# Kernel tuning notes

Hardware: AMD Instinct MI355X
Metric: run time of the kernel (lower is better)

## Reference

```python
import jax, jax.numpy as jnp
import numpy as np

T, HID = 2048, 4096
H = 32                 # num_heads
Q_LORA = 1536
KV_LORA = 512
D_NOPE = 128
D_ROPE = 64
D_QK = D_NOPE + D_ROPE  # 192
D_V = 128
EPS = 1e-6
THETA = 10000.0


def rmsnorm(x, scale):
    var = jnp.mean(x * x, axis=-1, keepdims=True)
    return x * jax.lax.rsqrt(var + EPS) * scale


def rope_interleaved(x, positions):
    # x: [T, h, D_ROPE], GPT-J interleaved style (rope_interleave=True -> not neox)
    half = D_ROPE // 2
    inv_freq = THETA ** (-jnp.arange(0, D_ROPE, 2, dtype=jnp.float32) / D_ROPE)  # [half]
    ang = positions.astype(jnp.float32)[:, None] * inv_freq[None, :]             # [T, half]
    cos = jnp.cos(ang)[:, None, :]
    sin = jnp.sin(ang)[:, None, :]
    x1 = x[..., 0::2]
    x2 = x[..., 1::2]
    o1 = x1 * cos - x2 * sin
    o2 = x1 * sin + x2 * cos
    return jnp.stack([o1, o2], axis=-1).reshape(x.shape)


def setup_inputs() -> dict:
    key = jax.random.key(0)
    ks = jax.random.split(key, 8)
    s = 0.02
    return {
        "hidden_states": jax.random.normal(ks[0], (T, HID), dtype=jnp.float32),
        "positions": jnp.arange(T, dtype=jnp.int32),
        "w_qa": jax.random.normal(ks[1], (HID, Q_LORA), dtype=jnp.float32) * s,
        "qa_ln_scale": jnp.ones((Q_LORA,), dtype=jnp.float32),
        "w_qb": jax.random.normal(ks[2], (Q_LORA, H * D_QK), dtype=jnp.float32) * s,
        "w_kva": jax.random.normal(ks[3], (HID, KV_LORA + D_ROPE), dtype=jnp.float32) * s,
        "kva_ln_scale": jnp.ones((KV_LORA,), dtype=jnp.float32),
        "w_uk": jax.random.normal(ks[4], (KV_LORA, H, D_NOPE), dtype=jnp.float32) * s,
        "w_uv": jax.random.normal(ks[5], (KV_LORA, H, D_V), dtype=jnp.float32) * s,
        "w_o": jax.random.normal(ks[6], (H * D_V, HID), dtype=jnp.float32) * s,
    }


def reference(hidden_states, positions, w_qa, qa_ln_scale, w_qb, w_kva,
              kva_ln_scale, w_uk, w_uv, w_o):
    # Q path: low-rank down-proj -> RMSNorm -> up-proj -> split nope/rope
    q_c = rmsnorm(hidden_states @ w_qa, qa_ln_scale)            # [T, Q_LORA]
    q = (q_c @ w_qb).reshape(T, H, D_QK)
    q_nope, q_rope = q[:, :, :D_NOPE], q[:, :, D_NOPE:]
    # KV path: joint down-proj -> split latent / rope key
    kv_a = hidden_states @ w_kva                                 # [T, KV_LORA + D_ROPE]
    compressed = rmsnorm(kv_a[:, :KV_LORA], kva_ln_scale)        # [T, KV_LORA]
    k_rope = kv_a[:, KV_LORA:][:, None, :]                       # [T, 1, D_ROPE]
    # partial RoPE on rope-dims only
    q_rope = rope_interleaved(q_rope, positions)
    k_rope = rope_interleaved(k_rope, positions)[:, 0, :]        # [T, D_ROPE]
    # Absorbed MQA: fold W_UK into Q, attend the shared latent
    ql_nope = jnp.einsum('thd,rhd->thr', q_nope, w_uk)           # [T, H, KV_LORA]
    scale = D_QK ** -0.5
    scores = (jnp.einsum('thr,sr->ths', ql_nope, compressed) +
              jnp.einsum('thd,sd->ths', q_rope, k_rope)) * scale # [T, H, T]
    causal = positions[:, None] >= positions[None, :]            # [T, T]
    scores = jnp.where(causal[:, None, :], scores, jnp.finfo(scores.dtype).min)
    probs = jax.nn.softmax(scores, axis=-1)
    o_latent = jnp.einsum('ths,sr->thr', probs, compressed)      # [T, H, KV_LORA]
    o_v = jnp.einsum('thr,rhd->thd', o_latent, w_uv)             # [T, H, D_V]
    out = o_v.reshape(T, H * D_V) @ w_o                          # [T, HID]
    return out
```

## Files before the change

### kernel.cpp

```cpp
#include <hip/hip_runtime.h>
#include <stdint.h>

typedef unsigned short u16;
typedef __attribute__((ext_vector_type(8))) short short8;
typedef __attribute__((ext_vector_type(4))) float floatx4;
typedef __attribute__((ext_vector_type(4))) unsigned short u16x4;

#define T_TOK 2048
#define NHEAD 32

__device__ __forceinline__ float bf2f(u16 u) { return __uint_as_float(((unsigned)u) << 16); }
__device__ __forceinline__ u16 f2bf(float f) {
    unsigned u = __float_as_uint(f);
    return (u16)((u + 0x7fffu + ((u >> 16) & 1u)) >> 16);
}

__device__ __forceinline__ floatx4 mfma16(short8 a, short8 b, floatx4 c) {
    return __builtin_amdgcn_mfma_f32_16x16x32_bf16(a, b, c, 0, 0, 0);
}

__global__ __launch_bounds__(256) void gemm_bt(
    const u16* __restrict__ A, const u16* __restrict__ B, void* __restrict__ Cp,
    int M, int N, int K, int lda, int ldb, int ldc,
    long sA, long sB, long sC, int c_bf16)
{
    __shared__ u16 As[128 * 32];
    __shared__ u16 Bs[128 * 32];
    const int z = blockIdx.z;
    A += (long)z * sA;
    B += (long)z * sB;
    const int tid  = threadIdx.x;
    const int wave = tid >> 6;
    const int lane = tid & 63;
    const long m0 = (long)blockIdx.y * 128;
    const long n0 = (long)blockIdx.x * 128;
    const int wm = (wave & 1) * 64;
    const int wn = (wave >> 1) * 64;
    const int lr = lane & 15;
    const int lk = (lane >> 4) * 8;

    const u16* Ag = A + (m0 + (tid >> 2)) * (long)lda + (tid & 3) * 8;
    const u16* Bg = B + (n0 + (tid >> 2)) * (long)ldb + (tid & 3) * 8;
    const long a64 = (long)64 * lda, b64 = (long)64 * ldb;

    floatx4 acc[4][4] = {};

    for (int k0 = 0; k0 < K; k0 += 32) {
        __syncthreads();
        __builtin_amdgcn_global_load_lds(
            (const __attribute__((address_space(1))) void*)(Ag + k0),
            (__attribute__((address_space(3))) void*)(As + wave * 512), 16, 0, 0);
        __builtin_amdgcn_global_load_lds(
            (const __attribute__((address_space(1))) void*)(Ag + k0 + a64),
            (__attribute__((address_space(3))) void*)(As + 2048 + wave * 512), 16, 0, 0);
        __builtin_amdgcn_global_load_lds(
            (const __attribute__((address_space(1))) void*)(Bg + k0),
            (__attribute__((address_space(3))) void*)(Bs + wave * 512), 16, 0, 0);
        __builtin_amdgcn_global_load_lds(
            (const __attribute__((address_space(1))) void*)(Bg + k0 + b64),
            (__attribute__((address_space(3))) void*)(Bs + 2048 + wave * 512), 16, 0, 0);
        __syncthreads();
        short8 af[4], bfr[4];
#pragma unroll
        for (int t = 0; t < 4; t++) {
            af[t]  = *(const short8*)&As[(wm + t * 16 + lr) * 32 + lk];
            bfr[t] = *(const short8*)&Bs[(wn + t * 16 + lr) * 32 + lk];
        }
#pragma unroll
        for (int mt = 0; mt < 4; mt++)
#pragma unroll
            for (int nt = 0; nt < 4; nt++)
                acc[mt][nt] = mfma16(af[mt], bfr[nt], acc[mt][nt]);
    }

    const int rbase = wm + (lane >> 4) * 4;
    if (c_bf16) {
        u16* C = (u16*)Cp + (long)z * sC;
#pragma unroll
        for (int mt = 0; mt < 4; mt++)
#pragma unroll
            for (int nt = 0; nt < 4; nt++)
#pragma unroll
                for (int r = 0; r < 4; r++) {
                    long row = m0 + rbase + mt * 16 + r;
                    long col = n0 + wn + nt * 16 + lr;
                    C[row * ldc + col] = f2bf(acc[mt][nt][r]);
                }
    } else {
        float* C = (float*)Cp + (long)z * sC;
#pragma unroll
        for (int mt = 0; mt < 4; mt++)
#pragma unroll
            for (int nt = 0; nt < 4; nt++)
#pragma unroll
                for (int r = 0; r < 4; r++) {
                    long row = m0 + rbase + mt * 16 + r;
                    long col = n0 + wn + nt * 16 + lr;
                    C[row * ldc + col] = acc[mt][nt][r];
                }
    }
}

#define ESCALE 0.10411754f

#define STAGE_K(CIDX)                                                          \
    {                                                                          \
        const u16* ksrc_ = Kp + (long)(CIDX) * 18432 + st_idx;                 \
        _Pragma("unroll")                                                      \
        for (int p_ = 0; p_ < 9; p_++)                                         \
            __builtin_amdgcn_global_load_lds(                                  \
                (const __attribute__((address_space(1))) void*)(ksrc_ + p_ * 2048), \
                (__attribute__((address_space(3))) void*)(Ks + st_idx + p_ * 2048), 16, 0, 0); \
    }
#define STAGE_V(CIDX)                                                          \
    {                                                                          \
        const u16* vsrc_ = Vp + (long)(CIDX) * 16384 + st_idx;                 \
        _Pragma("unroll")                                                      \
        for (int p_ = 0; p_ < 8; p_++)                                         \
            __builtin_amdgcn_global_load_lds(                                  \
                (const __attribute__((address_space(1))) void*)(vsrc_ + p_ * 2048), \
                (__attribute__((address_space(3))) void*)(Vs + st_idx + p_ * 2048), 16, 0, 0); \
    }

__global__ __launch_bounds__(256, 2) void flash_attn(
    const u16* __restrict__ Qp, const u16* __restrict__ Kp,
    const u16* __restrict__ Vp, u16* __restrict__ o_lat)
{
    __shared__ __align__(16) u16 Ks[18 * 1024];
    __shared__ __align__(16) u16 Vs[16 * 1024];
    __shared__ __align__(16) u16 Ps[64 * 40];
    __shared__ float ex[64];

    const int h = blockIdx.y;
    const int tid = threadIdx.x, wave = tid >> 6, lane = tid & 63;
    const int lr = lane & 15, hi = lane >> 4;
    const int wnp = wave * 128;

    const int st_idx = (wave << 9) + lane * 8;

    STAGE_K(0);
    STAGE_V(0);

    for (int half = 0; half < 2; half++) {
        const int qt = half ? (31 - (int)blockIdx.x) : (int)blockIdx.x;
        const int qb = qt * 64;
        const int nchunks = 2 * qt + 2;

        const u16* Qb = Qp + ((long)h * T_TOK + qb + wave * 16 + lr) * 576 + hi * 8;
        short8 qf[18];
#pragma unroll
        for (int s = 0; s < 18; s++)
            qf[s] = __builtin_nontemporal_load((const short8*)(Qb + s * 32));

        floatx4 oacc[4][8] = {};
        float l_part[4] = {};

        for (int c = 0; c < nchunks; c++) {
            const int jb = c * 32;
            __syncthreads();
            floatx4 sacc[2] = {};
#pragma unroll
            for (int s = 0; s < 18; s++) {
                short8 b0 = *(const short8*)(Ks + s * 1024 + lane * 8);
                short8 b1 = *(const short8*)(Ks + s * 1024 + 512 + lane * 8);
                sacc[0] = mfma16(qf[s], b0, sacc[0]);
                sacc[1] = mfma16(qf[s], b1, sacc[1]);
            }
            const int qg = qb + wave * 16 + hi * 4;
#pragma unroll
            for (int nt = 0; nt < 2; nt++) {
                const int kg = jb + nt * 16 + lr;
#pragma unroll
                for (int r = 0; r < 4; r++) {
                    float p = (kg <= qg + r) ? exp2f(sacc[nt][r] * ESCALE) : 0.0f;
                    l_part[r] += p;
                    Ps[(wave * 16 + hi * 4 + r) * 40 + nt * 16 + lr] = f2bf(p);
                }
            }
            __syncthreads();
            if (c + 1 < nchunks) STAGE_K(c + 1);
            short8 pa[4];
#pragma unroll
            for (int mt = 0; mt < 4; mt++)
                pa[mt] = *(const short8*)(Ps + (mt * 16 + lr) * 40 + hi * 8);
#pragma unroll
            for (int nt = 0; nt < 8; nt++) {
                short8 vb = *(const short8*)(Vs + (wave * 8 + nt) * 512 + lane * 8);
#pragma unroll
                for (int mt = 0; mt < 4; mt++)
                    oacc[mt][nt] = mfma16(pa[mt], vb, oacc[mt][nt]);
            }
            asm volatile("s_waitcnt lgkmcnt(0)" ::: "memory");
            __builtin_amdgcn_s_barrier();
            __builtin_amdgcn_sched_barrier(0);
            if (c + 1 < nchunks) {
                STAGE_V(c + 1);
            } else if (half == 0) {
                STAGE_K(0);
                STAGE_V(0);
            }
        }

#pragma unroll
        for (int r = 0; r < 4; r++) {
            float v = l_part[r];
            v += __shfl_xor(v, 1); v += __shfl_xor(v, 2);
            v += __shfl_xor(v, 4); v += __shfl_xor(v, 8);
            l_part[r] = v;
        }
        if (lr == 0) {
#pragma unroll
            for (int r = 0; r < 4; r++) ex[wave * 16 + hi * 4 + r] = l_part[r];
        }
        asm volatile("s_waitcnt lgkmcnt(0)" ::: "memory");
        __builtin_amdgcn_s_barrier();
        __builtin_amdgcn_sched_barrier(0);
        const long obase = (long)h * T_TOK + qb;
#pragma unroll
        for (int mt = 0; mt < 4; mt++)
#pragma unroll
            for (int r = 0; r < 4; r++) {
                const int row = mt * 16 + hi * 4 + r;
                const float inv = 1.0f / ex[row];
#pragma unroll
                for (int nt = 0; nt < 8; nt++)
                    __builtin_nontemporal_store(
                        f2bf(oacc[mt][nt][r] * inv),
                        o_lat + (obase + row) * 512 + wnp + nt * 16 + lr);
            }
    }
}

__global__ __launch_bounds__(256) void cast_bf16_k(const float* __restrict__ src,
                                                   u16* __restrict__ dst, long n)
{
    long i = ((long)blockIdx.x * 256 + threadIdx.x) * 4;
    if (i + 3 < n) {
        float4 v = *(const float4*)(src + i);
        u16x4 o = { f2bf(v.x), f2bf(v.y), f2bf(v.z), f2bf(v.w) };
        *(u16x4*)(dst + i) = o;
    }
}

__global__ void transpose_cast(const float* __restrict__ src, u16* __restrict__ dst,
                               int R, int C, int Cpad)
{
    __shared__ float tile[32][33];
    const int cb = blockIdx.x * 32, rb = blockIdx.y * 32;
    for (int i = threadIdx.y; i < 32; i += 8) {
        int r = rb + i, c = cb + threadIdx.x;
        tile[i][threadIdx.x] = (r < R && c < C) ? src[(long)r * C + c] : 0.0f;
    }
    __syncthreads();
    for (int i = threadIdx.y; i < 32; i += 8) {
        int c = cb + i, r = rb + threadIdx.x;
        if (c < Cpad && r < R) dst[(long)c * R + r] = f2bf(tile[threadIdx.x][i]);
    }
}

__global__ __launch_bounds__(256) void permute_wuv(const float* __restrict__ src,
                                                   u16* __restrict__ dst)
{
    int idx = blockIdx.x * 256 + threadIdx.x;
    int r = idx & 511;
    int hd = idx >> 9;
    int d = hd & 127, h = hd >> 7;
    dst[idx] = f2bf(src[(long)r * 4096 + h * 128 + d]);
}

__global__ __launch_bounds__(256) void rmsnorm_rows(const u16* __restrict__ in,
                                                    const float* __restrict__ gamma,
                                                    u16* __restrict__ out, int n, float invn)
{
    const long base = (long)blockIdx.x * n;
    const int tid = threadIdx.x, wave = tid >> 6, lane = tid & 63;
    __shared__ float red[4];
    float ss = 0.f;
    for (int i = tid; i < n; i += 256) { float x = bf2f(in[base + i]); ss += x * x; }
    for (int o = 32; o > 0; o >>= 1) ss += __shfl_xor(ss, o);
    if (lane == 0) red[wave] = ss;
    __syncthreads();
    ss = red[0] + red[1] + red[2] + red[3];
    const float r = rsqrtf(ss * invn + 1e-6f);
    for (int i = tid; i < n; i += 256) {
        float x = bf2f(in[base + i]);
        out[base + i] = f2bf(x * r * gamma[i]);
    }
}

__global__ __launch_bounds__(256) void kv_post(const u16* __restrict__ kva,
                                               const float* __restrict__ gamma,
                                               const int* __restrict__ pos,
                                               u16* __restrict__ Kp2, u16* __restrict__ Vp2)
{
    const int t = blockIdx.x;
    const long base = (long)t * 640;
    const int tid = threadIdx.x, wave = tid >> 6, lane = tid & 63;
    __shared__ float red[4];
    float ss = 0.f;
    for (int i = tid; i < 512; i += 256) { float x = bf2f(kva[base + i]); ss += x * x; }
    for (int o = 32; o > 0; o >>= 1) ss += __shfl_xor(ss, o);
    if (lane == 0) red[wave] = ss;
    __syncthreads();
    ss = red[0] + red[1] + red[2] + red[3];
    const float r = rsqrtf(ss * (1.0f / 512.0f) + 1e-6f);
    const int rr = t & 31, j = t >> 5;
    {
        const long vbase = (long)j * 16384;
        const int e = rr & 7, lhi = (rr >> 3) * 16;
        for (int i = tid; i < 512; i += 256) {
            float x = bf2f(kva[base + i]) * r * gamma[i];
            const int ct = i >> 4, l = lhi + (i & 15);
            Vp2[vbase + ct * 512 + l * 8 + e] = f2bf(x);
        }
    }
    if (tid < 72) {
        const int g  = tid;
        const int i0 = g * 8;
        const int s  = i0 >> 5, p = s >> 1, sb = s & 1, hi2 = (i0 & 31) >> 3;
        const int wv = sb * 2 + (rr >> 4);
        const int ln = (rr & 15) + 16 * hi2;
        const long gidx = (long)j * 18432 + p * 2048 + wv * 512 + ln * 8;
        short8 outv;
        if (g < 64) {
#pragma unroll
            for (int m = 0; m < 8; m++) {
                float x = bf2f(kva[base + i0 + m]) * r * gamma[i0 + m];
                ((u16*)&outv)[m] = f2bf(x);
            }
        } else {
#pragma unroll
            for (int q = 0; q < 4; q++) {
                int jj = ((i0 - 512) >> 1) + q;
                float invf = powf(10000.0f, -(float)jj / 32.0f);
                float ang = (float)pos[t] * invf;
                float sn, cs;
                sincosf(ang, &sn, &cs);
                float x1 = bf2f(kva[base + 512 + 2 * jj]);
                float x2 = bf2f(kva[base + 512 + 2 * jj + 1]);
                ((u16*)&outv)[2 * q]     = f2bf(x1 * cs - x2 * sn);
                ((u16*)&outv)[2 * q + 1] = f2bf(x1 * sn + x2 * cs);
            }
        }
        *(short8*)(Kp2 + gidx) = outv;
    }
}

__global__ __launch_bounds__(256) void rope_q(const u16* __restrict__ q,
                                              const int* __restrict__ pos,
                                              u16* __restrict__ Qp)
{
    int idx = blockIdx.x * 256 + threadIdx.x;
    int j = idx & 31;
    int h = (idx >> 5) & 31;
    int t = idx >> 10;
    float invf = powf(10000.0f, -(float)j / 32.0f);
    float ang = (float)pos[t] * invf;
    float sn, cs;
    sincosf(ang, &sn, &cs);
    long qb = (long)t * 6144 + h * 192 + 128 + 2 * j;
    float x1 = bf2f(q[qb]), x2 = bf2f(q[qb + 1]);
    long ob = (long)h * T_TOK * 576 + (long)t * 576 + 512 + 2 * j;
    Qp[ob]     = f2bf(x1 * cs - x2 * sn);
    Qp[ob + 1] = f2bf(x1 * sn + x2 * cs);
}

extern "C" void kernel_launch(void* const* d_in, const int* in_sizes, int n_in,
                              void* d_out, int out_size, void* d_ws, size_t ws_size,
                              hipStream_t stream)
{
    const float* hidden = (const float*)d_in[0];
    const int* positions = (const int*)d_in[1];
    const float* w_qa  = (const float*)d_in[2];
    const float* qa_g  = (const float*)d_in[3];
    const float* w_qb  = (const float*)d_in[4];
    const float* w_kva = (const float*)d_in[5];
    const float* kva_g = (const float*)d_in[6];
    const float* w_uk  = (const float*)d_in[7];
    const float* w_uv  = (const float*)d_in[8];
    const float* w_o   = (const float*)d_in[9];

    char* ws = (char*)d_ws;
    u16* o_lat   = (u16*)(ws + 0);
    u16* qc      = (u16*)(ws + 0);
    u16* q       = (u16*)(ws + 6291456);
    u16* hid_bf  = (u16*)(ws + 31457280);
    u16* wqa_t   = (u16*)(ws + 48234496);
    u16* qc_raw  = (u16*)(ws + 60817408);
    u16* wqb_t   = (u16*)(ws + 67108864);
    u16* wkva_t  = (u16*)(ws + 85983232);
    u16* wuk_b   = (u16*)(ws + 91226112);
    u16* wuv_t   = (u16*)(ws + 95420416);
    u16* wo_t    = (u16*)(ws + 99614720);
    u16* kva_raw = (u16*)(ws + 133169152);
    u16* Kp      = (u16*)(ws + 135790592);
    u16* Vp      = (u16*)(ws + 138149888);
    u16* Qp      = (u16*)(ws + 140247040);
    u16* o_v     = Qp;

    cast_bf16_k<<<8192, 256, 0, stream>>>(hidden, hid_bf, 8388608);
    transpose_cast<<<dim3(48, 128),  dim3(32, 8), 0, stream>>>(w_qa,  wqa_t,  4096, 1536, 1536);
    transpose_cast<<<dim3(192, 48),  dim3(32, 8), 0, stream>>>(w_qb,  wqb_t,  1536, 6144, 6144);
    transpose_cast<<<dim3(20, 128),  dim3(32, 8), 0, stream>>>(w_kva, wkva_t, 4096, 576,  640);
    cast_bf16_k<<<2048, 256, 0, stream>>>(w_uk, wuk_b, 2097152);
    permute_wuv<<<8192, 256, 0, stream>>>(w_uv, wuv_t);
    transpose_cast<<<dim3(128, 128), dim3(32, 8), 0, stream>>>(w_o,   wo_t,   4096, 4096, 4096);

    gemm_bt<<<dim3(12, 16, 1), 256, 0, stream>>>(hid_bf, wqa_t, qc_raw,
        2048, 1536, 4096, 4096, 4096, 1536, 0, 0, 0, 1);
    gemm_bt<<<dim3(5, 16, 1), 256, 0, stream>>>(hid_bf, wkva_t, kva_raw,
        2048, 640, 4096, 4096, 4096, 640, 0, 0, 0, 1);
    rmsnorm_rows<<<2048, 256, 0, stream>>>(qc_raw, qa_g, qc, 1536, 1.0f / 1536.0f);
    kv_post<<<2048, 256, 0, stream>>>(kva_raw, kva_g, positions, Kp, Vp);

    gemm_bt<<<dim3(48, 16, 1), 256, 0, stream>>>(qc, wqb_t, q,
        2048, 6144, 1536, 1536, 1536, 6144, 0, 0, 0, 1);
    rope_q<<<8192, 256, 0, stream>>>(q, positions, Qp);
    gemm_bt<<<dim3(4, 16, 32), 256, 0, stream>>>(q, wuk_b, Qp,
        2048, 512, 128, 6144, 4096, 576, 192, 128, (long)2048 * 576, 1);

    flash_attn<<<dim3(16, 32), 256, 0, stream>>>(Qp, Kp, Vp, o_lat);

    gemm_bt<<<dim3(1, 16, 32), 256, 0, stream>>>(o_lat, wuv_t, o_v,
        2048, 128, 512, 512, 512, 4096, (long)2048 * 512, 65536, 128, 1);
    gemm_bt<<<dim3(32, 16, 1), 256, 0, stream>>>(o_v, wo_t, d_out,
        2048, 4096, 4096, 4096, 4096, 4096, 0, 0, 0, 0);
}
```

Measured before the change: 890.2 us.

## Fuse weight prep into one kernel, merge down-projections with split-K, fuse norms

All cast, transpose and permute prep kernels are merged into one large launch selected by block index. The two down-projection GEMMs (w_qa and w_kva) share one concatenated transposed weight and run as a single GEMM with 2-way split-K, writing fp32 partials. A fused post kernel sums the partials, applies both RMSNorms and the k RoPE in one pass. powf is replaced by exp2f, and removing launches and using split-K is meant to raise occupancy, at the cost of extra fp32 partial traffic.

```diff
diff --git a/kernel.cpp b/kernel.cpp
--- a/kernel.cpp
+++ b/kernel.cpp
@@ -231,85 +231,90 @@
     }
 }
 
-__global__ __launch_bounds__(256) void cast_bf16_k(const float* __restrict__ src,
-                                                   u16* __restrict__ dst, long n)
-{
-    long i = ((long)blockIdx.x * 256 + threadIdx.x) * 4;
-    if (i + 3 < n) {
-        float4 v = *(const float4*)(src + i);
+__global__ __launch_bounds__(256) void mega_prep(
+    const float* __restrict__ hidden, const float* __restrict__ w_qa,
+    const float* __restrict__ w_kva, const float* __restrict__ w_qb,
+    const float* __restrict__ w_o, const float* __restrict__ w_uk,
+    const float* __restrict__ w_uv,
+    u16* __restrict__ hid_bf, u16* __restrict__ comb, u16* __restrict__ wqb_t,
+    u16* __restrict__ wo_t, u16* __restrict__ wuk_b, u16* __restrict__ wuv_t)
+{
+    __shared__ float tile[32][33];
+    const int bid = blockIdx.x, tid = threadIdx.x;
+
+    if (bid < 8192) {
+        long i = ((long)bid * 256 + tid) * 4;
+        float4 v = *(const float4*)(hidden + i);
         u16x4 o = { f2bf(v.x), f2bf(v.y), f2bf(v.z), f2bf(v.w) };
-        *(u16x4*)(dst + i) = o;
-    }
-}
-
-__global__ void transpose_cast(const float* __restrict__ src, u16* __restrict__ dst,
-                               int R, int C, int Cpad)
-{
-    __shared__ float tile[32][33];
-    const int cb = blockIdx.x * 32, rb = blockIdx.y * 32;
-    for (int i = threadIdx.y; i < 32; i += 8) {
-        int r = rb + i, c = cb + threadIdx.x;
-        tile[i][threadIdx.x] = (r < R && c < C) ? src[(long)r * C + c] : 0.0f;
+        *(u16x4*)(hid_bf + i) = o;
+        return;
+    }
+    if (bid < 10240) {
+        long i = ((long)(bid - 8192) * 256 + tid) * 4;
+        float4 v = *(const float4*)(w_uk + i);
+        u16x4 o = { f2bf(v.x), f2bf(v.y), f2bf(v.z), f2bf(v.w) };
+        *(u16x4*)(wuk_b + i) = o;
+        return;
+    }
+    if (bid < 18432) {
+        int idx = (bid - 10240) * 256 + tid;
+        int r = idx & 511;
+        int hd = idx >> 9;
+        int d = hd & 127, h = hd >> 7;
+        wuv_t[idx] = f2bf(w_uv[(long)r * 4096 + h * 128 + d]);
+        return;
+    }
+    const float* src; u16* dst; int R, C, Cpad, l, gw;
+    if (bid < 24576)      { l = bid - 18432; gw = 48;  src = w_qa;  dst = comb;                 R = 4096; C = 1536; Cpad = 1536; }
+    else if (bid < 27136) { l = bid - 24576; gw = 20;  src = w_kva; dst = comb + 1536 * 4096;   R = 4096; C = 576;  Cpad = 640;  }
+    else if (bid < 36352) { l = bid - 27136; gw = 192; src = w_qb;  dst = wqb_t;                R = 1536; C = 6144; Cpad = 6144; }
+    else                  { l = bid - 36352; gw = 128; src = w_o;   dst = wo_t;                 R = 4096; C = 4096; Cpad = 4096; }
+    const int cb = (l % gw) * 32, rb = (l / gw) * 32;
+    const int tx = tid & 31, ty = tid >> 5;
+    for (int i = ty; i < 32; i += 8) {
+        int r = rb + i, c = cb + tx;
+        tile[i][tx] = (r < R && c < C) ? src[(long)r * C + c] : 0.0f;
     }
     __syncthreads();
-    for (int i = threadIdx.y; i < 32; i += 8) {
-        int c = cb + i, r = rb + threadIdx.x;
-        if (c < Cpad && r < R) dst[(long)c * R + r] = f2bf(tile[threadIdx.x][i]);
-    }
-}
-
-__global__ __launch_bounds__(256) void permute_wuv(const float* __restrict__ src,
-                                                   u16* __restrict__ dst)
-{
-    int idx = blockIdx.x * 256 + threadIdx.x;
-    int r = idx & 511;
-    int hd = idx >> 9;
-    int d = hd & 127, h = hd >> 7;
-    dst[idx] = f2bf(src[(long)r * 4096 + h * 128 + d]);
-}
-
-__global__ __launch_bounds__(256) void rmsnorm_rows(const u16* __restrict__ in,
-                                                    const float* __restrict__ gamma,
-                                                    u16* __restrict__ out, int n, float invn)
-{
-    const long base = (long)blockIdx.x * n;
+    for (int i = ty; i < 32; i += 8) {
+        int c = cb + i, r = rb + tx;
+        if (c < Cpad && r < R) dst[(long)c * R + r] = f2bf(tile[tx][i]);
+    }
+}
+
+__global__ __launch_bounds__(256) void post_stage1(
+    const float* __restrict__ p0, const float* __restrict__ p1,
+    const float* __restrict__ qa_g, const float* __restrict__ kva_g,
+    const int* __restrict__ pos,
+    u16* __restrict__ qc, u16* __restrict__ Kp2, u16* __restrict__ Vp2)
+{
+    const int t = blockIdx.x;
     const int tid = threadIdx.x, wave = tid >> 6, lane = tid & 63;
-    __shared__ float red[4];
-    float ss = 0.f;
-    for (int i = tid; i < n; i += 256) { float x = bf2f(in[base + i]); ss += x * x; }
-    for (int o = 32; o > 0; o >>= 1) ss += __shfl_xor(ss, o);
-    if (lane == 0) red[wave] = ss;
+    __shared__ float row[2176];
+    __shared__ float red1[4], red2[4];
+    const long b = (long)t * 2176;
+    float s1 = 0.f, s2 = 0.f;
+    for (int i = tid; i < 2176; i += 256) {
+        float v = p0[b + i] + p1[b + i];
+        row[i] = v;
+        if (i < 1536) s1 += v * v;
+        else if (i < 2048) s2 += v * v;
+    }
+    for (int o = 32; o > 0; o >>= 1) { s1 += __shfl_xor(s1, o); s2 += __shfl_xor(s2, o); }
+    if (lane == 0) { red1[wave] = s1; red2[wave] = s2; }
     __syncthreads();
-    ss = red[0] + red[1] + red[2] + red[3];
-    const float r = rsqrtf(ss * invn + 1e-6f);
-    for (int i = tid; i < n; i += 256) {
-        float x = bf2f(in[base + i]);
-        out[base + i] = f2bf(x * r * gamma[i]);
-    }
-}
-
-__global__ __launch_bounds__(256) void kv_post(const u16* __restrict__ kva,
-                                               const float* __restrict__ gamma,
-                                               const int* __restrict__ pos,
-                                               u16* __restrict__ Kp2, u16* __restrict__ Vp2)
-{
-    const int t = blockIdx.x;
-    const long base = (long)t * 640;
-    const int tid = threadIdx.x, wave = tid >> 6, lane = tid & 63;
-    __shared__ float red[4];
-    float ss = 0.f;
-    for (int i = tid; i < 512; i += 256) { float x = bf2f(kva[base + i]); ss += x * x; }
-    for (int o = 32; o > 0; o >>= 1) ss += __shfl_xor(ss, o);
-    if (lane == 0) red[wave] = ss;
-    __syncthreads();
-    ss = red[0] + red[1] + red[2] + red[3];
-    const float r = rsqrtf(ss * (1.0f / 512.0f) + 1e-6f);
+    s1 = red1[0] + red1[1] + red1[2] + red1[3];
+    s2 = red2[0] + red2[1] + red2[2] + red2[3];
+    const float r1 = rsqrtf(s1 * (1.0f / 1536.0f) + 1e-6f);
+    const float r2 = rsqrtf(s2 * (1.0f / 512.0f) + 1e-6f);
+    for (int i = tid; i < 1536; i += 256)
+        qc[(long)t * 1536 + i] = f2bf(row[i] * r1 * qa_g[i]);
     const int rr = t & 31, j = t >> 5;
     {
         const long vbase = (long)j * 16384;
         const int e = rr & 7, lhi = (rr >> 3) * 16;
         for (int i = tid; i < 512; i += 256) {
-            float x = bf2f(kva[base + i]) * r * gamma[i];
+            float x = row[1536 + i] * r2 * kva_g[i];
             const int ct = i >> 4, l = lhi + (i & 15);
             Vp2[vbase + ct * 512 + l * 8 + e] = f2bf(x);
         }
@@ -324,22 +329,20 @@
         short8 outv;
         if (g < 64) {
 #pragma unroll
-            for (int m = 0; m < 8; m++) {
-                float x = bf2f(kva[base + i0 + m]) * r * gamma[i0 + m];
-                ((u16*)&outv)[m] = f2bf(x);
-            }
+            for (int m = 0; m < 8; m++)
+                ((u16*)&outv)[m] = f2bf(row[1536 + i0 + m] * r2 * kva_g[i0 + m]);
         } else {
 #pragma unroll
-            for (int q = 0; q < 4; q++) {
-                int jj = ((i0 - 512) >> 1) + q;
-                float invf = powf(10000.0f, -(float)jj / 32.0f);
+            for (int q_ = 0; q_ < 4; q_++) {
+                int jj = ((i0 - 512) >> 1) + q_;
+                float invf = exp2f(-(float)jj * 0.4152410119f);
                 float ang = (float)pos[t] * invf;
                 float sn, cs;
                 sincosf(ang, &sn, &cs);
-                float x1 = bf2f(kva[base + 512 + 2 * jj]);
-                float x2 = bf2f(kva[base + 512 + 2 * jj + 1]);
-                ((u16*)&outv)[2 * q]     = f2bf(x1 * cs - x2 * sn);
-                ((u16*)&outv)[2 * q + 1] = f2bf(x1 * sn + x2 * cs);
+                float x1 = row[2048 + 2 * jj];
+                float x2 = row[2048 + 2 * jj + 1];
+                ((u16*)&outv)[2 * q_]     = f2bf(x1 * cs - x2 * sn);
+                ((u16*)&outv)[2 * q_ + 1] = f2bf(x1 * sn + x2 * cs);
             }
         }
         *(short8*)(Kp2 + gidx) = outv;
@@ -354,7 +357,7 @@
     int j = idx & 31;
     int h = (idx >> 5) & 31;
     int t = idx >> 10;
-    float invf = powf(10000.0f, -(float)j / 32.0f);
+    float invf = exp2f(-(float)j * 0.4152410119f);
     float ang = (float)pos[t] * invf;
     float sn, cs;
     sincosf(ang, &sn, &cs);
@@ -381,37 +384,28 @@
     const float* w_o   = (const float*)d_in[9];
 
     char* ws = (char*)d_ws;
-    u16* o_lat   = (u16*)(ws + 0);
-    u16* qc      = (u16*)(ws + 0);
-    u16* q       = (u16*)(ws + 6291456);
-    u16* hid_bf  = (u16*)(ws + 31457280);
-    u16* wqa_t   = (u16*)(ws + 48234496);
-    u16* qc_raw  = (u16*)(ws + 60817408);
-    u16* wqb_t   = (u16*)(ws + 67108864);
-    u16* wkva_t  = (u16*)(ws + 85983232);
-    u16* wuk_b   = (u16*)(ws + 91226112);
-    u16* wuv_t   = (u16*)(ws + 95420416);
-    u16* wo_t    = (u16*)(ws + 99614720);
-    u16* kva_raw = (u16*)(ws + 133169152);
-    u16* Kp      = (u16*)(ws + 135790592);
-    u16* Vp      = (u16*)(ws + 138149888);
-    u16* Qp      = (u16*)(ws + 140247040);
-    u16* o_v     = Qp;
-
-    cast_bf16_k<<<8192, 256, 0, stream>>>(hidden, hid_bf, 8388608);
-    transpose_cast<<<dim3(48, 128),  dim3(32, 8), 0, stream>>>(w_qa,  wqa_t,  4096, 1536, 1536);
-    transpose_cast<<<dim3(192, 48),  dim3(32, 8), 0, stream>>>(w_qb,  wqb_t,  1536, 6144, 6144);
-    transpose_cast<<<dim3(20, 128),  dim3(32, 8), 0, stream>>>(w_kva, wkva_t, 4096, 576,  640);
-    cast_bf16_k<<<2048, 256, 0, stream>>>(w_uk, wuk_b, 2097152);
-    permute_wuv<<<8192, 256, 0, stream>>>(w_uv, wuv_t);
-    transpose_cast<<<dim3(128, 128), dim3(32, 8), 0, stream>>>(w_o,   wo_t,   4096, 4096, 4096);
-
-    gemm_bt<<<dim3(12, 16, 1), 256, 0, stream>>>(hid_bf, wqa_t, qc_raw,
-        2048, 1536, 4096, 4096, 4096, 1536, 0, 0, 0, 1);
-    gemm_bt<<<dim3(5, 16, 1), 256, 0, stream>>>(hid_bf, wkva_t, kva_raw,
-        2048, 640, 4096, 4096, 4096, 640, 0, 0, 0, 1);
-    rmsnorm_rows<<<2048, 256, 0, stream>>>(qc_raw, qa_g, qc, 1536, 1.0f / 1536.0f);
-    kv_post<<<2048, 256, 0, stream>>>(kva_raw, kva_g, positions, Kp, Vp);
+    u16*   hid_bf = (u16*)(ws + 0);
+    u16*   qc     = (u16*)(ws + 0);
+    u16*   comb   = (u16*)(ws + 16777216);
+    u16*   q      = (u16*)(ws + 16777216);
+    float* p0     = (float*)(ws + 34603008);
+    float* p1     = (float*)(ws + 52428800);
+    u16*   o_lat  = (u16*)(ws + 0);
+    u16*   wqb_t  = (u16*)(ws + 70254592);
+    u16*   wuk_b  = (u16*)(ws + 89128960);
+    u16*   wuv_t  = (u16*)(ws + 93323264);
+    u16*   wo_t   = (u16*)(ws + 97517568);
+    u16*   Kp     = (u16*)(ws + 131072000);
+    u16*   Vp     = (u16*)(ws + 133431296);
+    u16*   Qp     = (u16*)(ws + 135528448);
+    u16*   o_v    = Qp;
+
+    mega_prep<<<52736, 256, 0, stream>>>(hidden, w_qa, w_kva, w_qb, w_o, w_uk, w_uv,
+                                         hid_bf, comb, wqb_t, wo_t, wuk_b, wuv_t);
+
+    gemm_bt<<<dim3(17, 16, 2), 256, 0, stream>>>(hid_bf, comb, p0,
+        2048, 2176, 2048, 4096, 4096, 2176, 2048, 2048, (long)2048 * 2176, 0);
+    post_stage1<<<2048, 256, 0, stream>>>(p0, p1, qa_g, kva_g, positions, qc, Kp, Vp);
 
     gemm_bt<<<dim3(48, 16, 1), 256, 0, stream>>>(qc, wqb_t, q,
         2048, 6144, 1536, 1536, 1536, 6144, 0, 0, 0, 1);
```

New measurement: 725.9 us. 18.5% less time.
